# Optimization experiments

Measured on AMD Instinct MI355X. Metric: run time of the kernel, lower is better.

## Reference

```python
import jax, jax.numpy as jnp
import numpy as np

START_AGE = 0
END_AGE = 100
LAMBDA_1 = 0.2
LAMBDA_2 = 0.05
EPS = 1e-3

N = 524288
WIDTH = END_AGE + 1 - START_AGE  # 101


def setup_inputs() -> dict:
    key = jax.random.key(0)
    k1, k2 = jax.random.split(key)
    inp = jax.random.normal(k1, (N, WIDTH), dtype=jnp.float32)
    target = jax.random.randint(k2, (N,), 0, WIDTH, dtype=jnp.int32)
    return {"input": inp, "target": target}


def reference(input, target):
    # softmax over age bins
    p = jax.nn.softmax(input, axis=1)                                  # [N, W]
    a = jnp.arange(START_AGE, END_AGE + 1, dtype=jnp.float32)          # [W]
    tf = target.astype(jnp.float32)
    # expected age per sample
    mean = jnp.sum(p * a, axis=1)                                      # [N]
    mean_loss = jnp.mean((mean - tf) ** 2) / 2.0
    # vectorized one-hot gather: prob of ground-truth bin
    prob_gt = jnp.take_along_axis(p, target[:, None].astype(jnp.int32), axis=1)  # [N,1]
    # mask of bins with prob strictly below the GT prob; detached in the original
    mask = jax.lax.stop_gradient((p < prob_gt).astype(p.dtype))        # [N, W]
    p_not_K = mask * p
    residue_loss = jnp.mean(jnp.sum(-(p_not_K + EPS) * jnp.log(p_not_K + EPS), axis=1))
    batch_average_K = jnp.sum(mask == 0).astype(jnp.float32) / N
    return (LAMBDA_1 * mean_loss, LAMBDA_2 * residue_loss, batch_average_K)
```

## Files before the change

### kernel.cpp

```cpp
#include <hip/hip_runtime.h>

#define N_ROWS   524288
#define W_BINS   101
#define EPS_F    1e-3f
#define RPB      64
#define NBLK     (N_ROWS / RPB)
#define TILE_F   (RPB * W_BINS)

typedef const float __attribute__((address_space(1)))* gptr_t;
typedef float __attribute__((address_space(3)))* sptr_t;

__global__ __launch_bounds__(64) void mrl_main(const float* __restrict__ x,
                                               const int* __restrict__ tgt,
                                               float4* __restrict__ partial) {
    __shared__ float sm[TILE_F];
    const int lane = threadIdx.x;
    const float* gbase = x + (size_t)blockIdx.x * TILE_F;

    #pragma unroll
    for (int q = 0; q < 25; ++q) {
        __builtin_amdgcn_global_load_lds((gptr_t)(gbase + q * 256 + lane * 4),
                                         (sptr_t)(sm + q * 256), 16, 0, 0);
    }
    if (lane < 16) {
        __builtin_amdgcn_global_load_lds((gptr_t)(gbase + 6400 + lane * 4),
                                         (sptr_t)(sm + 6400), 16, 0, 0);
    }

    const int row = blockIdx.x * RPB + lane;
    const int t   = tgt[row];

    __syncthreads();

    const float* r = sm + lane * W_BINS;

    float se0 = 0.f, se1 = 0.f, sa0 = 0.f, sa1 = 0.f;
    #pragma unroll
    for (int i = 0; i < 100; i += 2) {
        float e0 = __expf(r[i]);
        float e1 = __expf(r[i + 1]);
        se0 += e0; sa0 += e0 * (float)i;
        se1 += e1; sa1 += e1 * (float)(i + 1);
    }
    {
        float e = __expf(r[100]);
        se0 += e; sa0 += e * 100.0f;
    }
    const float se  = se0 + se1;
    const float sea = sa0 + sa1;

    const float egt = __expf(r[t]);
    const float inv = __builtin_amdgcn_rcpf(se);
    const float d   = sea * inv - (float)t;
    float sq = d * d;

    float rc0 = 0.f, rc1 = 0.f;
    int   k   = 0;
    #pragma unroll
    for (int i = 0; i < 100; i += 2) {
        float e0 = __expf(r[i]);
        float e1 = __expf(r[i + 1]);
        bool  l0 = e0 < egt, l1 = e1 < egt;
        float q0 = (l0 ? e0 * inv : 0.f) + EPS_F;
        float q1 = (l1 ? e1 * inv : 0.f) + EPS_F;
        rc0 -= q0 * __logf(q0);
        rc1 -= q1 * __logf(q1);
        k   += (l0 ? 0 : 1) + (l1 ? 0 : 1);
    }
    {
        float e = __expf(r[100]);
        bool  l = e < egt;
        float q = (l ? e * inv : 0.f) + EPS_F;
        rc0 -= q * __logf(q);
        k   += l ? 0 : 1;
    }
    float rc = rc0 + rc1;
    float kf = (float)k;

    #pragma unroll
    for (int off = 32; off >= 1; off >>= 1) {
        sq += __shfl_xor(sq, off);
        rc += __shfl_xor(rc, off);
        kf += __shfl_xor(kf, off);
    }
    if (lane == 0) {
        partial[blockIdx.x] = make_float4(sq, rc, kf, 0.0f);
    }
}

__global__ __launch_bounds__(256) void mrl_reduce(const float4* __restrict__ partial,
                                                  float* __restrict__ out) {
    double s = 0.0, r = 0.0, k = 0.0;
    for (int i = threadIdx.x; i < NBLK; i += 256) {
        float4 v = partial[i];
        s += (double)v.x; r += (double)v.y; k += (double)v.z;
    }
    #pragma unroll
    for (int off = 32; off >= 1; off >>= 1) {
        s += __shfl_xor(s, off);
        r += __shfl_xor(r, off);
        k += __shfl_xor(k, off);
    }
    __shared__ double sd[12];
    const int w = threadIdx.x >> 6;
    if ((threadIdx.x & 63) == 0) { sd[w * 3 + 0] = s; sd[w * 3 + 1] = r; sd[w * 3 + 2] = k; }
    __syncthreads();
    if (threadIdx.x == 0) {
        double S = sd[0] + sd[3] + sd[6] + sd[9];
        double R = sd[1] + sd[4] + sd[7] + sd[10];
        double K = sd[2] + sd[5] + sd[8] + sd[11];
        const double n = (double)N_ROWS;
        out[0] = (float)(0.1  * (S / n));
        out[1] = (float)(0.05 * (R / n));
        out[2] = (float)(K / n);
    }
}

extern "C" void kernel_launch(void* const* d_in, const int* in_sizes, int n_in,
                              void* d_out, int out_size, void* d_ws, size_t ws_size,
                              hipStream_t stream) {
    const float* x   = (const float*)d_in[0];
    const int*   tgt = (const int*)d_in[1];
    float*  out     = (float*)d_out;
    float4* partial = (float4*)d_ws;

    mrl_main<<<NBLK, RPB, 0, stream>>>(x, tgt, partial);
    mrl_reduce<<<1, 256, 0, stream>>>(partial, out);
}
```

Before: 302.6 us.

## Use persistent blocks with double-buffered LDS DMA to overlap loads and compute

Replaces the one-tile-per-block launch with a fixed grid of 1024 single-wave blocks. Each block walks 8 tiles and prefetches the next tile's inputs and targets into a second LDS buffer through global_load_lds. It waits with an explicit vmcnt so the next batch's loads stay in flight while the current tile is computed. This aims to hide global-memory latency inside a wave rather than depending on many resident blocks. The cost is that LDS use per block doubles, which lowers how many blocks fit on a CU and may leave a tail wave of blocks. Correctness also relies on the hand-written vmcnt count matching the number of issued loads.

```diff
diff --git a/kernel.cpp b/kernel.cpp
--- a/kernel.cpp
+++ b/kernel.cpp
@@ -4,94 +4,123 @@
 #define W_BINS   101
 #define EPS_F    1e-3f
 #define RPB      64
-#define NBLK     (N_ROWS / RPB)
+#define NTILES   (N_ROWS / RPB)
+#define GRID     1024
+#define TPB      (NTILES / GRID)
 #define TILE_F   (RPB * W_BINS)
 
-typedef const float __attribute__((address_space(1)))* gptr_t;
-typedef float __attribute__((address_space(3)))* sptr_t;
+typedef const float __attribute__((address_space(1)))* gfp_t;
+typedef float __attribute__((address_space(3)))* sfp_t;
+typedef const int __attribute__((address_space(1)))* gip_t;
+typedef int __attribute__((address_space(3)))* sip_t;
+
+#define WAIT_VM27() asm volatile("s_waitcnt vmcnt(27)" ::: "memory")
+#define WAIT_VM0()  asm volatile("s_waitcnt vmcnt(0)"  ::: "memory")
+
+__device__ __forceinline__ void dma_batch(const float* gsrc, float* lds,
+                                          const int* gt, int* lt, int lane) {
+    #pragma unroll
+    for (int q = 0; q < 25; ++q) {
+        __builtin_amdgcn_global_load_lds((gfp_t)(gsrc + q * 256 + lane * 4),
+                                         (sfp_t)(lds + q * 256), 16, 0, 0);
+    }
+    if (lane < 16) {
+        __builtin_amdgcn_global_load_lds((gfp_t)(gsrc + 6400 + lane * 4),
+                                         (sfp_t)(lds + 6400), 16, 0, 0);
+        __builtin_amdgcn_global_load_lds((gip_t)(gt + lane * 4),
+                                         (sip_t)lt, 16, 0, 0);
+    }
+}
 
 __global__ __launch_bounds__(64) void mrl_main(const float* __restrict__ x,
                                                const int* __restrict__ tgt,
                                                float4* __restrict__ partial) {
-    __shared__ float sm[TILE_F];
+    __shared__ float sm[2][TILE_F];
+    __shared__ int   ts[2][RPB];
     const int lane = threadIdx.x;
-    const float* gbase = x + (size_t)blockIdx.x * TILE_F;
 
-    #pragma unroll
-    for (int q = 0; q < 25; ++q) {
-        __builtin_amdgcn_global_load_lds((gptr_t)(gbase + q * 256 + lane * 4),
-                                         (sptr_t)(sm + q * 256), 16, 0, 0);
+    int tile = blockIdx.x;
+    dma_batch(x + (size_t)tile * TILE_F, sm[0], tgt + tile * RPB, ts[0], lane);
+
+    float racc = 0.f, sqac = 0.f, kfac = 0.f;
+    int buf = 0;
+
+    #pragma unroll 1
+    for (int j = 0; j < TPB; ++j) {
+        if (j + 1 < TPB) {
+            const int nt = tile + GRID;
+            dma_batch(x + (size_t)nt * TILE_F, sm[buf ^ 1],
+                      tgt + nt * RPB, ts[buf ^ 1], lane);
+            WAIT_VM27();
+        } else {
+            WAIT_VM0();
+        }
+
+        const float* r = sm[buf] + lane * W_BINS;
+        const int    t = ts[buf][lane];
+
+        float se0 = 0.f, se1 = 0.f, sa0 = 0.f, sa1 = 0.f;
+        #pragma unroll
+        for (int i = 0; i < 100; i += 2) {
+            float e0 = __expf(r[i]);
+            float e1 = __expf(r[i + 1]);
+            se0 += e0; sa0 += e0 * (float)i;
+            se1 += e1; sa1 += e1 * (float)(i + 1);
+        }
+        {
+            float e = __expf(r[100]);
+            se0 += e; sa0 += e * 100.0f;
+        }
+        const float se  = se0 + se1;
+        const float sea = sa0 + sa1;
+
+        const float egt = __expf(r[t]);
+        const float inv = __builtin_amdgcn_rcpf(se);
+        const float d   = sea * inv - (float)t;
+        sqac += d * d;
+
+        float rc0 = 0.f, rc1 = 0.f;
+        int   kk  = 0;
+        #pragma unroll
+        for (int i = 0; i < 100; i += 2) {
+            float e0 = __expf(r[i]);
+            float e1 = __expf(r[i + 1]);
+            bool  l0 = e0 < egt, l1 = e1 < egt;
+            float q0 = (l0 ? e0 * inv : 0.f) + EPS_F;
+            float q1 = (l1 ? e1 * inv : 0.f) + EPS_F;
+            rc0 -= q0 * __logf(q0);
+            rc1 -= q1 * __logf(q1);
+            kk  += (l0 ? 0 : 1) + (l1 ? 0 : 1);
+        }
+        {
+            float e = __expf(r[100]);
+            bool  l = e < egt;
+            float q = (l ? e * inv : 0.f) + EPS_F;
+            rc0 -= q * __logf(q);
+            kk  += l ? 0 : 1;
+        }
+        racc += rc0 + rc1;
+        kfac += (float)kk;
+
+        tile += GRID;
+        buf ^= 1;
     }
-    if (lane < 16) {
-        __builtin_amdgcn_global_load_lds((gptr_t)(gbase + 6400 + lane * 4),
-                                         (sptr_t)(sm + 6400), 16, 0, 0);
-    }
-
-    const int row = blockIdx.x * RPB + lane;
-    const int t   = tgt[row];
-
-    __syncthreads();
-
-    const float* r = sm + lane * W_BINS;
-
-    float se0 = 0.f, se1 = 0.f, sa0 = 0.f, sa1 = 0.f;
-    #pragma unroll
-    for (int i = 0; i < 100; i += 2) {
-        float e0 = __expf(r[i]);
-        float e1 = __expf(r[i + 1]);
-        se0 += e0; sa0 += e0 * (float)i;
-        se1 += e1; sa1 += e1 * (float)(i + 1);
-    }
-    {
-        float e = __expf(r[100]);
-        se0 += e; sa0 += e * 100.0f;
-    }
-    const float se  = se0 + se1;
-    const float sea = sa0 + sa1;
-
-    const float egt = __expf(r[t]);
-    const float inv = __builtin_amdgcn_rcpf(se);
-    const float d   = sea * inv - (float)t;
-    float sq = d * d;
-
-    float rc0 = 0.f, rc1 = 0.f;
-    int   k   = 0;
-    #pragma unroll
-    for (int i = 0; i < 100; i += 2) {
-        float e0 = __expf(r[i]);
-        float e1 = __expf(r[i + 1]);
-        bool  l0 = e0 < egt, l1 = e1 < egt;
-        float q0 = (l0 ? e0 * inv : 0.f) + EPS_F;
-        float q1 = (l1 ? e1 * inv : 0.f) + EPS_F;
-        rc0 -= q0 * __logf(q0);
-        rc1 -= q1 * __logf(q1);
-        k   += (l0 ? 0 : 1) + (l1 ? 0 : 1);
-    }
-    {
-        float e = __expf(r[100]);
-        bool  l = e < egt;
-        float q = (l ? e * inv : 0.f) + EPS_F;
-        rc0 -= q * __logf(q);
-        k   += l ? 0 : 1;
-    }
-    float rc = rc0 + rc1;
-    float kf = (float)k;
 
     #pragma unroll
     for (int off = 32; off >= 1; off >>= 1) {
-        sq += __shfl_xor(sq, off);
-        rc += __shfl_xor(rc, off);
-        kf += __shfl_xor(kf, off);
+        sqac += __shfl_xor(sqac, off);
+        racc += __shfl_xor(racc, off);
+        kfac += __shfl_xor(kfac, off);
     }
     if (lane == 0) {
-        partial[blockIdx.x] = make_float4(sq, rc, kf, 0.0f);
+        partial[blockIdx.x] = make_float4(sqac, racc, kfac, 0.0f);
     }
 }
 
 __global__ __launch_bounds__(256) void mrl_reduce(const float4* __restrict__ partial,
                                                   float* __restrict__ out) {
     double s = 0.0, r = 0.0, k = 0.0;
-    for (int i = threadIdx.x; i < NBLK; i += 256) {
+    for (int i = threadIdx.x; i < GRID; i += 256) {
         float4 v = partial[i];
         s += (double)v.x; r += (double)v.y; k += (double)v.z;
     }
@@ -124,6 +153,6 @@
     float*  out     = (float*)d_out;
     float4* partial = (float4*)d_ws;
 
-    mrl_main<<<NBLK, RPB, 0, stream>>>(x, tgt, partial);
+    mrl_main<<<GRID, 64, 0, stream>>>(x, tgt, partial);
     mrl_reduce<<<1, 256, 0, stream>>>(partial, out);
 }
```

New measurement: 329.2 us. +8.8%, slower.

## Load rows directly from global into registers and cache exponentials

Applied to the files above, without the earlier changes.

Drops the LDS staging through global_load_lds. Each thread now reads its own 101-float row straight from global memory, and the 101 exponentials are kept in a register array so the second pass does not recompute them. Blocks grow to 256 threads with a launch-bounds occupancy hint, and the reduction now reads one partial per wavefront. Per-thread row reads are strided by 404 bytes, so global accesses are uncoalesced, and the 101-entry register array may raise register pressure or spill.

```diff
diff --git a/kernel.cpp b/kernel.cpp
--- a/kernel.cpp
+++ b/kernel.cpp
@@ -3,79 +3,64 @@
 #define N_ROWS   524288
 #define W_BINS   101
 #define EPS_F    1e-3f
-#define RPB      64
-#define NBLK     (N_ROWS / RPB)
-#define TILE_F   (RPB * W_BINS)
+#define NTHREADS 256
+#define NBLK     (N_ROWS / NTHREADS)
+#define NWAVES   (N_ROWS / 64)
 
-typedef const float __attribute__((address_space(1)))* gptr_t;
-typedef float __attribute__((address_space(3)))* sptr_t;
+__global__ __launch_bounds__(256, 3) void mrl_main(const float* __restrict__ x,
+                                                   const int* __restrict__ tgt,
+                                                   float4* __restrict__ partial) {
+    const int row = blockIdx.x * NTHREADS + threadIdx.x;
+    const float* __restrict__ r = x + (size_t)row * W_BINS;
 
-__global__ __launch_bounds__(64) void mrl_main(const float* __restrict__ x,
-                                               const int* __restrict__ tgt,
-                                               float4* __restrict__ partial) {
-    __shared__ float sm[TILE_F];
-    const int lane = threadIdx.x;
-    const float* gbase = x + (size_t)blockIdx.x * TILE_F;
+    const int   t  = tgt[row];
+    const float xt = r[t];
 
-    #pragma unroll
-    for (int q = 0; q < 25; ++q) {
-        __builtin_amdgcn_global_load_lds((gptr_t)(gbase + q * 256 + lane * 4),
-                                         (sptr_t)(sm + q * 256), 16, 0, 0);
-    }
-    if (lane < 16) {
-        __builtin_amdgcn_global_load_lds((gptr_t)(gbase + 6400 + lane * 4),
-                                         (sptr_t)(sm + 6400), 16, 0, 0);
-    }
-
-    const int row = blockIdx.x * RPB + lane;
-    const int t   = tgt[row];
-
-    __syncthreads();
-
-    const float* r = sm + lane * W_BINS;
-
+    float e[W_BINS];
     float se0 = 0.f, se1 = 0.f, sa0 = 0.f, sa1 = 0.f;
     #pragma unroll
     for (int i = 0; i < 100; i += 2) {
-        float e0 = __expf(r[i]);
-        float e1 = __expf(r[i + 1]);
-        se0 += e0; sa0 += e0 * (float)i;
-        se1 += e1; sa1 += e1 * (float)(i + 1);
+        float v0 = r[i];
+        float v1 = r[i + 1];
+        float E0 = __expf(v0);
+        float E1 = __expf(v1);
+        e[i] = E0;     e[i + 1] = E1;
+        se0 += E0;     sa0 += E0 * (float)i;
+        se1 += E1;     sa1 += E1 * (float)(i + 1);
     }
     {
-        float e = __expf(r[100]);
-        se0 += e; sa0 += e * 100.0f;
+        float E = __expf(r[100]);
+        e[100] = E;
+        se0 += E; sa0 += E * 100.0f;
     }
     const float se  = se0 + se1;
     const float sea = sa0 + sa1;
 
-    const float egt = __expf(r[t]);
+    const float egt = __expf(xt);
     const float inv = __builtin_amdgcn_rcpf(se);
     const float d   = sea * inv - (float)t;
     float sq = d * d;
 
     float rc0 = 0.f, rc1 = 0.f;
-    int   k   = 0;
+    int   kk  = 0;
     #pragma unroll
     for (int i = 0; i < 100; i += 2) {
-        float e0 = __expf(r[i]);
-        float e1 = __expf(r[i + 1]);
-        bool  l0 = e0 < egt, l1 = e1 < egt;
-        float q0 = (l0 ? e0 * inv : 0.f) + EPS_F;
-        float q1 = (l1 ? e1 * inv : 0.f) + EPS_F;
+        bool  l0 = e[i]     < egt;
+        bool  l1 = e[i + 1] < egt;
+        float q0 = (l0 ? e[i]     * inv : 0.f) + EPS_F;
+        float q1 = (l1 ? e[i + 1] * inv : 0.f) + EPS_F;
         rc0 -= q0 * __logf(q0);
         rc1 -= q1 * __logf(q1);
-        k   += (l0 ? 0 : 1) + (l1 ? 0 : 1);
+        kk  += (l0 ? 0 : 1) + (l1 ? 0 : 1);
     }
     {
-        float e = __expf(r[100]);
-        bool  l = e < egt;
-        float q = (l ? e * inv : 0.f) + EPS_F;
+        bool  l = e[100] < egt;
+        float q = (l ? e[100] * inv : 0.f) + EPS_F;
         rc0 -= q * __logf(q);
-        k   += l ? 0 : 1;
+        kk  += l ? 0 : 1;
     }
     float rc = rc0 + rc1;
-    float kf = (float)k;
+    float kf = (float)kk;
 
     #pragma unroll
     for (int off = 32; off >= 1; off >>= 1) {
@@ -83,15 +68,15 @@
         rc += __shfl_xor(rc, off);
         kf += __shfl_xor(kf, off);
     }
-    if (lane == 0) {
-        partial[blockIdx.x] = make_float4(sq, rc, kf, 0.0f);
+    if ((threadIdx.x & 63) == 0) {
+        partial[row >> 6] = make_float4(sq, rc, kf, 0.0f);
     }
 }
 
 __global__ __launch_bounds__(256) void mrl_reduce(const float4* __restrict__ partial,
                                                   float* __restrict__ out) {
     double s = 0.0, r = 0.0, k = 0.0;
-    for (int i = threadIdx.x; i < NBLK; i += 256) {
+    for (int i = threadIdx.x; i < NWAVES; i += 256) {
         float4 v = partial[i];
         s += (double)v.x; r += (double)v.y; k += (double)v.z;
     }
@@ -124,6 +109,6 @@
     float*  out     = (float*)d_out;
     float4* partial = (float4*)d_ws;
 
-    mrl_main<<<NBLK, RPB, 0, stream>>>(x, tgt, partial);
+    mrl_main<<<NBLK, NTHREADS, 0, stream>>>(x, tgt, partial);
     mrl_reduce<<<1, 256, 0, stream>>>(partial, out);
 }
```

Result: slower. 322.9 us (+6.7%).
